# Optimization experiments

Hardware: AMD Instinct MI355X
Metric: run time of the kernel (lower is better)

## Reference

```python
import jax, jax.numpy as jnp
import numpy as np

S, B, D, H = 2048, 16, 1024, 1024


def setup_inputs() -> dict:
    key = jax.random.key(0)
    k1, k2, k3 = jax.random.split(key, 3)
    X = jax.random.normal(k1, (S, B, D), dtype=jnp.float32)
    hidden = jax.random.normal(k2, (B, H), dtype=jnp.float32)
    W = jax.random.normal(k3, (3 * H, D), dtype=jnp.float32) * 0.02  # nn.Linear weight [out,in]
    b = jnp.zeros((3 * H,), dtype=jnp.float32)
    return {"X": X, "hidden": hidden, "W": W, "b": b}


def reference(X, hidden, W, b):
    # window=1: source = X. Linear projection -> Z, F, O chunks.
    Y = jnp.einsum('sbd,hd->sbh', X, W) + b  # [S,B,3H]
    Z, F, O = jnp.split(Y, 3, axis=2)
    Z = jnp.tanh(Z)
    F = jax.nn.sigmoid(F)

    # ForgetMult recurrence: C_t = F_t * C_{t-1} + (1 - F_t) * Z_t, C_0 = hidden
    def step(c, fz):
        f, z = fz
        c = f * c + (1.0 - f) * z
        return c, c

    _, C = jax.lax.scan(step, hidden, (F, Z))  # C: [S,B,H]
    Hout = jax.nn.sigmoid(O) * C
    return Hout, C[-1:, :, :]
```

## Files before the change

kernel.cpp:

```cpp
#include <hip/hip_runtime.h>
#include <hip/hip_bf16.h>
#include <stdint.h>

#define S_LEN 2048
#define B_SZ  16
#define D_DIM 1024
#define H_DIM 1024
#define M_TOT (S_LEN * B_SZ)
#define N_TOT (3 * H_DIM)
#define K_TOT D_DIM

#define BM 256
#define BN 256
#define BK 64
#define NT   (K_TOT / BK)
#define NTN  (N_TOT / BN)
#define NWG  ((M_TOT / BM) * NTN)

#define NCHUNK 32
#define CLEN   64
#define NCH    (B_SZ * H_DIM)

typedef __attribute__((ext_vector_type(8))) short short8;
typedef __attribute__((ext_vector_type(4))) float f32x4;

__device__ __forceinline__ void gload_lds16(const void* g, void* l) {
  __builtin_amdgcn_global_load_lds((__attribute__((address_space(1))) void*)g,
                                   (__attribute__((address_space(3))) void*)l,
                                   16, 0, 0);
}

__device__ __forceinline__ unsigned short f2bfbits(float x) {
  union { __hip_bfloat16 h; unsigned short u; } cv;
  cv.h = __float2bfloat16(x);
  return cv.u;
}

__device__ __forceinline__ float sigmoidf_fast(float y) {
  return 1.f / (1.f + __expf(-y));
}

__device__ __forceinline__ float tanhf_fast(float y) {
  float ay = fabsf(y);
  float e  = __expf(-2.f * ay);
  float t  = (1.f - e) / (1.f + e);
  return copysignf(t, y);
}

__global__ void cvt_kernel(const float* __restrict__ in,
                           unsigned short* __restrict__ out, int n4) {
  int i = blockIdx.x * 256 + threadIdx.x;
  if (i < n4) {
    float4 v = ((const float4*)in)[i];
    ushort4 o;
    o.x = f2bfbits(v.x); o.y = f2bfbits(v.y);
    o.z = f2bfbits(v.z); o.w = f2bfbits(v.w);
    ((ushort4*)out)[i] = o;
  }
}

__global__ __launch_bounds__(512, 2) void gemm_act(
    const __hip_bfloat16* __restrict__ Xb,
    const __hip_bfloat16* __restrict__ Wb,
    const float* __restrict__ bias,
    unsigned short* __restrict__ wsZ,
    unsigned short* __restrict__ wsF,
    unsigned short* __restrict__ wsO) {
  __shared__ __align__(16) char lds[131072];

  int bid = blockIdx.x;
  int swz = (bid & 7) * (NWG >> 3) + (bid >> 3);
  int tm  = swz / NTN;
  int tn  = swz - tm * NTN;
  const int m0 = tm * BM;
  const int n0 = tn * BN;

  const int tid  = threadIdx.x;
  const int lane = tid & 63;
  const int wid  = tid >> 6;
  const int wr   = wid >> 2;
  const int wc   = wid & 3;
  const int lr   = lane & 15;
  const int lg   = lane >> 4;

  const int srow  = tid >> 3;
  const int sslot = tid & 7;

  const char* Ab = (const char*)(Xb + (size_t)m0 * K_TOT);
  const char* Bb = (const char*)(Wb + (size_t)n0 * K_TOT);

  f32x4 acc[8][4];
  const f32x4 vz = {0.f, 0.f, 0.f, 0.f};
  #pragma unroll
  for (int m = 0; m < 8; ++m)
    #pragma unroll
    for (int n = 0; n < 4; ++n) acc[m][n] = vz;

  #define STAGE(t)                                                            \
    {                                                                         \
      const size_t kb = (size_t)(t) * (BK * 2);                               \
      char* la = lds + ((t) & 1) * 32768;                                     \
      char* lb = lds + 65536 + ((t) & 1) * 32768;                             \
      _Pragma("unroll")                                                       \
      for (int h = 0; h < 4; ++h) {                                           \
        int r = h * 64 + srow;                                                \
        gload_lds16(Ab + (size_t)r * (K_TOT * 2) + kb + ((sslot ^ (r & 7)) << 4), \
                    la + r * 128 + (sslot << 4));                             \
      }                                                                       \
      _Pragma("unroll")                                                       \
      for (int h = 0; h < 4; ++h) {                                           \
        int r = h * 64 + srow;                                                \
        gload_lds16(Bb + (size_t)r * (K_TOT * 2) + kb + ((sslot ^ (r & 7)) << 4), \
                    lb + r * 128 + (sslot << 4));                             \
      }                                                                       \
    }

  STAGE(0);

  for (int t = 0; t < NT; ++t) {
    if (t + 1 < NT) {
      STAGE(t + 1);
      asm volatile("s_waitcnt vmcnt(8)" ::: "memory");
    } else {
      asm volatile("s_waitcnt vmcnt(0)" ::: "memory");
    }
    __builtin_amdgcn_s_barrier();

    const char* la = lds + (t & 1) * 32768;
    const char* lb = lds + 65536 + (t & 1) * 32768;

    short8 bfr[4][2];
    #pragma unroll
    for (int n = 0; n < 4; ++n)
      #pragma unroll
      for (int ks = 0; ks < 2; ++ks) {
        int row = wc * 64 + n * 16 + lr;
        bfr[n][ks] = *(const short8*)(lb + row * 128 + ((((ks << 2) | lg) ^ (row & 7)) << 4));
      }

    #pragma unroll
    for (int q = 0; q < 4; ++q) {
      short8 afr[2][2];
      #pragma unroll
      for (int mm = 0; mm < 2; ++mm)
        #pragma unroll
        for (int ks = 0; ks < 2; ++ks) {
          int row = wr * 128 + (q * 2 + mm) * 16 + lr;
          afr[mm][ks] = *(const short8*)(la + row * 128 + ((((ks << 2) | lg) ^ (row & 7)) << 4));
        }
      __builtin_amdgcn_s_setprio(1);
      #pragma unroll
      for (int ks = 0; ks < 2; ++ks)
        #pragma unroll
        for (int mm = 0; mm < 2; ++mm)
          #pragma unroll
          for (int n = 0; n < 4; ++n)
            acc[q * 2 + mm][n] = __builtin_amdgcn_mfma_f32_16x16x32_bf16(
                afr[mm][ks], bfr[n][ks], acc[q * 2 + mm][n], 0, 0, 0);
      __builtin_amdgcn_s_setprio(0);
      asm volatile("" ::: "memory");
      __builtin_amdgcn_s_barrier();
    }
  }

  const int chunk = n0 >> 10;
  const int hbase = (n0 & (H_DIM - 1)) + wc * 64;
  unsigned short* dst = (chunk == 0) ? wsZ : (chunk == 1) ? wsF : wsO;

  char* ep = lds + wid * 16384;
  float bv[4];
  #pragma unroll
  for (int n = 0; n < 4; ++n) bv[n] = bias[n0 + wc * 64 + n * 16 + lr];

  #pragma unroll
  for (int m = 0; m < 8; ++m)
    #pragma unroll
    for (int n = 0; n < 4; ++n)
      #pragma unroll
      for (int r = 0; r < 4; ++r) {
        float y = acc[m][n][r] + bv[n];
        float v = (chunk == 0) ? tanhf_fast(y) : sigmoidf_fast(y);
        int rowl = m * 16 + lg * 4 + r;
        *(unsigned short*)(ep + rowl * 128 + ((n * 16 + lr) << 1)) = f2bfbits(v);
      }

  #pragma unroll
  for (int it = 0; it < 16; ++it) {
    int rl = it * 8 + (lane >> 3);
    short8 v = *(const short8*)(ep + rl * 128 + ((lane & 7) << 4));
    size_t grow = (size_t)(m0 + wr * 128 + rl);
    *(short8*)((char*)dst + (grow * H_DIM + hbase) * 2 + ((lane & 7) << 4)) = v;
  }
}

__global__ void scan_pass1(const __hip_bfloat16* __restrict__ F,
                           const __hip_bfloat16* __restrict__ Z,
                           float* __restrict__ chP, float* __restrict__ chA) {
  int t  = blockIdx.x * 256 + threadIdx.x;
  int ch = t & (NCH - 1);
  int c  = t >> 14;
  size_t base = (size_t)c * CLEN * NCH + ch;
  float P = 1.f, A = 0.f;
  #pragma unroll 8
  for (int i = 0; i < CLEN; ++i) {
    float f = __bfloat162float(F[base + (size_t)i * NCH]);
    float z = __bfloat162float(Z[base + (size_t)i * NCH]);
    A = fmaf(f, A, (1.f - f) * z);
    P *= f;
  }
  chP[t] = P;
  chA[t] = A;
}

__global__ void scan_mid(const float* __restrict__ chP, const float* __restrict__ chA,
                         const float* __restrict__ hidden,
                         float* __restrict__ Cst, float* __restrict__ outLast) {
  int ch = blockIdx.x * 256 + threadIdx.x;
  float c0 = hidden[ch];
  #pragma unroll
  for (int c = 0; c < NCHUNK; ++c) {
    Cst[c * NCH + ch] = c0;
    c0 = fmaf(chP[c * NCH + ch], c0, chA[c * NCH + ch]);
  }
  outLast[ch] = c0;
}

__global__ void scan_pass2(const __hip_bfloat16* __restrict__ F,
                           const __hip_bfloat16* __restrict__ Z,
                           const __hip_bfloat16* __restrict__ O,
                           const float* __restrict__ Cst,
                           float* __restrict__ out) {
  int t  = blockIdx.x * 256 + threadIdx.x;
  int ch = t & (NCH - 1);
  int c  = t >> 14;
  float C = Cst[c * NCH + ch];
  size_t base = (size_t)c * CLEN * NCH + ch;
  #pragma unroll 8
  for (int i = 0; i < CLEN; ++i) {
    size_t idx = base + (size_t)i * NCH;
    float f = __bfloat162float(F[idx]);
    float z = __bfloat162float(Z[idx]);
    C = fmaf(f, C, (1.f - f) * z);
    out[idx] = __bfloat162float(O[idx]) * C;
  }
}

extern "C" void kernel_launch(void* const* d_in, const int* in_sizes, int n_in,
                              void* d_out, int out_size, void* d_ws, size_t ws_size,
                              hipStream_t stream) {
  const float* X      = (const float*)d_in[0];
  const float* hidden = (const float*)d_in[1];
  const float* W      = (const float*)d_in[2];
  const float* bias   = (const float*)d_in[3];
  float* out = (float*)d_out;

  char* ws = (char*)d_ws;
  __hip_bfloat16* Xb  = (__hip_bfloat16*)(ws);
  __hip_bfloat16* Wb  = (__hip_bfloat16*)(ws + 67108864);
  unsigned short* wsZ = (unsigned short*)(ws + 73400320);
  unsigned short* wsF = (unsigned short*)(ws + 140509184);
  unsigned short* wsO = (unsigned short*)(ws + 207618048);
  float* chP = (float*)(ws + 274726912);
  float* chA = (float*)(ws + 276824064);
  float* Cst = (float*)(ws + 278921216);

  cvt_kernel<<<(M_TOT * K_TOT / 4 + 255) / 256, 256, 0, stream>>>(X, (unsigned short*)Xb, M_TOT * K_TOT / 4);
  cvt_kernel<<<(N_TOT * K_TOT / 4 + 255) / 256, 256, 0, stream>>>(W, (unsigned short*)Wb, N_TOT * K_TOT / 4);

  gemm_act<<<NWG, 512, 0, stream>>>(Xb, Wb, bias, wsZ, wsF, wsO);

  scan_pass1<<<(NCHUNK * NCH) / 256, 256, 0, stream>>>(
      (const __hip_bfloat16*)wsF, (const __hip_bfloat16*)wsZ, chP, chA);
  scan_mid<<<NCH / 256, 256, 0, stream>>>(chP, chA, hidden, Cst, out + (size_t)M_TOT * H_DIM);
  scan_pass2<<<(NCHUNK * NCH) / 256, 256, 0, stream>>>(
      (const __hip_bfloat16*)wsF, (const __hip_bfloat16*)wsZ,
      (const __hip_bfloat16*)wsO, Cst, out);
}
```

Baseline: 400.8 us.

## Split K-tile LDS into 32-wide halves and restructure GEMM mainloop into quadrant schedule

```diff
diff --git a/kernel.cpp b/kernel.cpp
--- a/kernel.cpp
+++ b/kernel.cpp
@@ -82,9 +82,10 @@
   const int wc   = wid & 3;
   const int lr   = lane & 15;
   const int lg   = lane >> 4;
-
-  const int srow  = tid >> 3;
-  const int sslot = tid & 7;
+  const int psl  = (lg ^ (lr & 3)) << 4;
+
+  const int srow  = tid >> 2;
+  const int ssl   = ((tid & 3) ^ (srow & 3)) << 4;
 
   const char* Ab = (const char*)(Xb + (size_t)m0 * K_TOT);
   const char* Bb = (const char*)(Wb + (size_t)n0 * K_TOT);
@@ -96,71 +97,103 @@
     #pragma unroll
     for (int n = 0; n < 4; ++n) acc[m][n] = vz;
 
-  #define STAGE(t)                                                            \
+  #define STAGE_HALF(gbase, ldsoff, tt, ks)                                   \
     {                                                                         \
-      const size_t kb = (size_t)(t) * (BK * 2);                               \
-      char* la = lds + ((t) & 1) * 32768;                                     \
-      char* lb = lds + 65536 + ((t) & 1) * 32768;                             \
+      char* l = lds + (ldsoff) + ((((tt) & 1) << 1) | (ks)) * 16384;          \
+      const size_t kb = ((size_t)(tt) * 64 + (ks) * 32) * 2;                  \
       _Pragma("unroll")                                                       \
-      for (int h = 0; h < 4; ++h) {                                           \
-        int r = h * 64 + srow;                                                \
-        gload_lds16(Ab + (size_t)r * (K_TOT * 2) + kb + ((sslot ^ (r & 7)) << 4), \
-                    la + r * 128 + (sslot << 4));                             \
-      }                                                                       \
-      _Pragma("unroll")                                                       \
-      for (int h = 0; h < 4; ++h) {                                           \
-        int r = h * 64 + srow;                                                \
-        gload_lds16(Bb + (size_t)r * (K_TOT * 2) + kb + ((sslot ^ (r & 7)) << 4), \
-                    lb + r * 128 + (sslot << 4));                             \
+      for (int j = 0; j < 2; ++j) {                                           \
+        int r = j * 128 + srow;                                               \
+        gload_lds16((gbase) + (size_t)r * (K_TOT * 2) + kb + ssl,             \
+                    l + j * 8192 + tid * 16);                                 \
       }                                                                       \
     }
 
-  STAGE(0);
+  #define BAR()                                                               \
+    { asm volatile("" ::: "memory");                                          \
+      __builtin_amdgcn_s_barrier();                                           \
+      asm volatile("" ::: "memory"); }
+
+  #define LGKM0()                                                             \
+    { asm volatile("s_waitcnt lgkmcnt(0)" ::: "memory");                      \
+      __builtin_amdgcn_sched_barrier(0); }
+
+  #define VM0()                                                               \
+    { asm volatile("s_waitcnt vmcnt(0)" ::: "memory");                        \
+      __builtin_amdgcn_sched_barrier(0); }
+
+  #define READ_A(dst, tb, mh)                                                 \
+    _Pragma("unroll")                                                         \
+    for (int mm = 0; mm < 4; ++mm)                                            \
+      _Pragma("unroll")                                                       \
+      for (int ks = 0; ks < 2; ++ks) {                                        \
+        int row = wr * 128 + (mh) * 64 + mm * 16 + lr;                        \
+        dst[mm][ks] = *(const short8*)(lds + (((tb) << 1) | ks) * 16384 +     \
+                                       row * 64 + psl);                       \
+      }
+
+  #define READ_B(dst, tb, nh)                                                 \
+    _Pragma("unroll")                                                         \
+    for (int nn = 0; nn < 2; ++nn)                                            \
+      _Pragma("unroll")                                                       \
+      for (int ks = 0; ks < 2; ++ks) {                                        \
+        int row = wc * 64 + (nh) * 32 + nn * 16 + lr;                         \
+        dst[nn][ks] = *(const short8*)(lds + 65536 +                          \
+                                       (((tb) << 1) | ks) * 16384 +           \
+                                       row * 64 + psl);                       \
+      }
+
+  #define MFMA_Q(mh, nh, A, Bf)                                               \
+    __builtin_amdgcn_s_setprio(1);                                            \
+    _Pragma("unroll")                                                         \
+    for (int ks = 0; ks < 2; ++ks)                                            \
+      _Pragma("unroll")                                                       \
+      for (int mm = 0; mm < 4; ++mm)                                          \
+        _Pragma("unroll")                                                     \
+        for (int nn = 0; nn < 2; ++nn)                                        \
+          acc[(mh) * 4 + mm][(nh) * 2 + nn] =                                 \
+              __builtin_amdgcn_mfma_f32_16x16x32_bf16(                        \
+                  A[mm][ks], Bf[nn][ks], acc[(mh) * 4 + mm][(nh) * 2 + nn],   \
+                  0, 0, 0);                                                   \
+    __builtin_amdgcn_s_setprio(0);
+
+  STAGE_HALF(Ab, 0, 0, 0);
+  STAGE_HALF(Ab, 0, 0, 1);
+  STAGE_HALF(Bb, 65536, 0, 0);
+  STAGE_HALF(Bb, 65536, 0, 1);
+  VM0();
+  BAR();
+
+  short8 afr[4][2], bfr0[2][2], bfr1[2][2];
 
   for (int t = 0; t < NT; ++t) {
+    const int tb = t & 1;
     if (t + 1 < NT) {
-      STAGE(t + 1);
-      asm volatile("s_waitcnt vmcnt(8)" ::: "memory");
-    } else {
-      asm volatile("s_waitcnt vmcnt(0)" ::: "memory");
+      STAGE_HALF(Ab, 0, t + 1, 0);
+      STAGE_HALF(Ab, 0, t + 1, 1);
+      STAGE_HALF(Bb, 65536, t + 1, 0);
+      STAGE_HALF(Bb, 65536, t + 1, 1);
     }
-    __builtin_amdgcn_s_barrier();
-
-    const char* la = lds + (t & 1) * 32768;
-    const char* lb = lds + 65536 + (t & 1) * 32768;
-
-    short8 bfr[4][2];
-    #pragma unroll
-    for (int n = 0; n < 4; ++n)
-      #pragma unroll
-      for (int ks = 0; ks < 2; ++ks) {
-        int row = wc * 64 + n * 16 + lr;
-        bfr[n][ks] = *(const short8*)(lb + row * 128 + ((((ks << 2) | lg) ^ (row & 7)) << 4));
-      }
-
-    #pragma unroll
-    for (int q = 0; q < 4; ++q) {
-      short8 afr[2][2];
-      #pragma unroll
-      for (int mm = 0; mm < 2; ++mm)
-        #pragma unroll
-        for (int ks = 0; ks < 2; ++ks) {
-          int row = wr * 128 + (q * 2 + mm) * 16 + lr;
-          afr[mm][ks] = *(const short8*)(la + row * 128 + ((((ks << 2) | lg) ^ (row & 7)) << 4));
-        }
-      __builtin_amdgcn_s_setprio(1);
-      #pragma unroll
-      for (int ks = 0; ks < 2; ++ks)
-        #pragma unroll
-        for (int mm = 0; mm < 2; ++mm)
-          #pragma unroll
-          for (int n = 0; n < 4; ++n)
-            acc[q * 2 + mm][n] = __builtin_amdgcn_mfma_f32_16x16x32_bf16(
-                afr[mm][ks], bfr[n][ks], acc[q * 2 + mm][n], 0, 0, 0);
-      __builtin_amdgcn_s_setprio(0);
-      asm volatile("" ::: "memory");
-      __builtin_amdgcn_s_barrier();
-    }
+    READ_A(afr, tb, 0);
+    READ_B(bfr0, tb, 0);
+    BAR();
+    LGKM0();
+    MFMA_Q(0, 0, afr, bfr0);
+    BAR();
+    READ_B(bfr1, tb, 1);
+    BAR();
+    LGKM0();
+    MFMA_Q(0, 1, afr, bfr1);
+    BAR();
+    READ_A(afr, tb, 1);
+    BAR();
+    LGKM0();
+    MFMA_Q(1, 1, afr, bfr1);
+    BAR();
+    VM0();
+    BAR();
+    MFMA_Q(1, 0, afr, bfr0);
+    BAR();
   }
 
   const int chunk = n0 >> 10;
```

Result: slower. 428.0 us (+6.8%).
